# Kernel optimization log

Measured on AMD Instinct MI355X. Metric: run time of the kernel, lower is better.

## Reference

```python
import jax, jax.numpy as jnp
import numpy as np

B, S, D, H = 4, 2048, 1024, 16
HD = D // H  # head_dim = 64


def setup_inputs() -> dict:
    key = jax.random.key(0)
    k_x, k_m, k_wi, k_bi, k_wo, k_bo = jax.random.split(key, 6)
    x = jax.random.normal(k_x, (B, S, D), dtype=jnp.float32)
    mask = jax.random.randint(k_m, (B, S), 0, 2, dtype=jnp.int32)
    # Keras Dense: kernel shape (in, out), glorot-ish scale; bias zeros-ish (random small here)
    w_in = jax.random.normal(k_wi, (D, 3 * D), dtype=jnp.float32) * (1.0 / np.sqrt(D))
    b_in = jax.random.normal(k_bi, (3 * D,), dtype=jnp.float32) * 0.02
    w_out = jax.random.normal(k_wo, (D, D), dtype=jnp.float32) * (1.0 / np.sqrt(D))
    b_out = jax.random.normal(k_bo, (D,), dtype=jnp.float32) * 0.02
    return {"x": x, "w_in": w_in, "b_in": b_in, "w_out": w_out, "b_out": b_out, "mask": mask}


def reference(x, w_in, b_in, w_out, b_out, mask):
    b, s, _ = x.shape
    scale = jnp.asarray(HD ** (-0.5), dtype=x.dtype)
    qkv = x @ w_in + b_in                              # (B, S, 3D)
    qkv = qkv.reshape(b, s, 3, H, HD).transpose(2, 0, 3, 1, 4)  # (3, B, H, S, HD)
    q, k, v = qkv[0], qkv[1], qkv[2]
    q = q * scale
    attn = jnp.einsum("bhqd,bhkd->bhqk", q, k)         # (B, H, S, S)
    neg_inf = jnp.asarray(float("-inf"), dtype=attn.dtype)
    attn_mask = jnp.where(mask[:, None, None, :] > 0, jnp.zeros((), attn.dtype), neg_inf)
    attn = jax.nn.softmax(attn + attn_mask, axis=-1)
    out = jnp.einsum("bhqk,bhkd->bhqd", attn, v)        # (B, H, S, HD)
    out = out.transpose(0, 2, 1, 3).reshape(b, s, D)
    return out @ w_out + b_out
```

## Files before the change

### kernel.cpp

```cpp
#include <hip/hip_runtime.h>

#define B_  4
#define S_  2048
#define D_  1024
#define H_  16
#define HD_ 64
#define BH_ (B_*H_)

typedef _Float16 h16;
typedef _Float16 h4 __attribute__((ext_vector_type(4)));
typedef _Float16 h8 __attribute__((ext_vector_type(8)));
typedef float    f32x4 __attribute__((ext_vector_type(4)));

__device__ __forceinline__ void gload16(const h16* g, h16* l) {
  __builtin_amdgcn_global_load_lds(
      (const __attribute__((address_space(1))) unsigned int*)g,
      (__attribute__((address_space(3))) unsigned int*)l, 16, 0, 0);
}

__global__ void maskscan_k(const int* __restrict__ mask,
                           int* __restrict__ posmap, int* __restrict__ nvalid) {
  __shared__ int partial[256];
  int b = blockIdx.x;
  const int* mb = mask + b * S_;
  int t = threadIdx.x;
  int base = t * 8;
  int loc[8], cnt = 0;
#pragma unroll
  for (int j = 0; j < 8; j++) { loc[j] = cnt; cnt += (mb[base + j] != 0); }
  partial[t] = cnt;
  __syncthreads();
  for (int off = 1; off < 256; off <<= 1) {
    int v = (t >= off) ? partial[t - off] : 0;
    __syncthreads();
    partial[t] += v;
    __syncthreads();
  }
  int excl = (t == 0) ? 0 : partial[t - 1];
#pragma unroll
  for (int j = 0; j < 8; j++)
    posmap[b * S_ + base + j] = (mb[base + j] != 0) ? (excl + loc[j]) : -1;
  if (t == 255) nvalid[b] = partial[255];
}

__global__ void convert_k(const float* __restrict__ in, h16* __restrict__ out,
                          int n) {
  int idx = (blockIdx.x * 256 + threadIdx.x) * 8;
  if (idx + 8 <= n) {
    float4 f0 = *(const float4*)(in + idx);
    float4 f1 = *(const float4*)(in + idx + 4);
    h16 t[8] = {(h16)f0.x, (h16)f0.y, (h16)f0.z, (h16)f0.w,
                (h16)f1.x, (h16)f1.y, (h16)f1.z, (h16)f1.w};
    *(h8*)(out + idx) = *(h8*)t;
  } else {
    for (int j = idx; j < n; j++) out[j] = (h16)in[j];
  }
}

__global__ void transpose_conv_k(const float* __restrict__ in,
                                 h16* __restrict__ out, int R, int C) {
  __shared__ h16 tile[32][33];
  int bx = blockIdx.x * 32;
  int by = blockIdx.y * 32;
  int tx = threadIdx.x, ty = threadIdx.y;
#pragma unroll
  for (int i = 0; i < 32; i += 8)
    tile[ty + i][tx] = (h16)in[(size_t)(by + ty + i) * C + bx + tx];
  __syncthreads();
#pragma unroll
  for (int i = 0; i < 32; i += 8)
    out[(size_t)(bx + ty + i) * R + by + tx] = tile[tx][ty + i];
}

template <int MODE>
__global__ __launch_bounds__(256)
void gemm_bt(const h16* __restrict__ A, const h16* __restrict__ BT,
             const h16* __restrict__ bias, const int* __restrict__ posmap,
             void* __restrict__ out0v, h16* __restrict__ out1,
             h16* __restrict__ out2, int M, int N, int K) {
  const int tid  = threadIdx.x;
  const int lane = tid & 63;
  const int w    = tid >> 6;
  const int quad = lane >> 4;
  const int l16  = lane & 15;
  const int m0   = blockIdx.x * 128;
  const int n0   = blockIdx.y * 128;

  __shared__ alignas(16) h16 As[128 * 32];
  __shared__ alignas(16) h16 Bs[128 * 32];

  const f32x4 zero = {0.f, 0.f, 0.f, 0.f};
  f32x4 acc[4][4];
#pragma unroll
  for (int i = 0; i < 4; i++)
#pragma unroll
    for (int j = 0; j < 4; j++) acc[i][j] = zero;

  const int wm = (w >> 1) * 64;
  const int wn = (w & 1) * 64;
  const int srow = (lane >> 2);
  const int sko  = (lane & 3) * 8;

  for (int kt = 0; kt < K; kt += 32) {
#pragma unroll
    for (int c = 0; c < 2; c++) {
      int chunk = w * 2 + c;
      int row = chunk * 16 + srow;
      gload16(&A[(size_t)(m0 + row) * K + kt + sko], &As[chunk * 512]);
      gload16(&BT[(size_t)(n0 + row) * K + kt + sko], &Bs[chunk * 512]);
    }
    __syncthreads();
    h8 af[4], bfr[4];
#pragma unroll
    for (int i = 0; i < 4; i++)
      af[i] = *(const h8*)(&As[(wm + i * 16 + l16) * 32 + quad * 8]);
#pragma unroll
    for (int j = 0; j < 4; j++)
      bfr[j] = *(const h8*)(&Bs[(wn + j * 16 + l16) * 32 + quad * 8]);
#pragma unroll
    for (int i = 0; i < 4; i++)
#pragma unroll
      for (int j = 0; j < 4; j++)
        acc[i][j] = __builtin_amdgcn_mfma_f32_16x16x32_f16(af[i], bfr[j],
                                                           acc[i][j], 0, 0, 0);
    __syncthreads();
  }

#pragma unroll
  for (int i = 0; i < 4; i++) {
#pragma unroll
    for (int j = 0; j < 4; j++) {
      int n = n0 + wn + j * 16 + l16;
      float bv = (float)bias[n];
#pragma unroll
      for (int r = 0; r < 4; r++) {
        int m = m0 + wm + i * 16 + quad * 4 + r;
        float v = acc[i][j][r] + bv;
        if (MODE == 0) {
          h16* q0 = (h16*)out0v;
          int which = n >> 10;
          int h  = (n >> 6) & 15;
          int hd = n & 63;
          int b  = m >> 11;
          int s  = m & 2047;
          if (which == 0) {
            q0[(((size_t)(b * 16 + h)) * S_ + s) * HD_ + hd] = (h16)(v * 0.125f);
          } else {
            int pos = posmap[b * S_ + s];
            if (pos >= 0) {
              if (which == 1)
                out1[(((size_t)(b * 16 + h)) * S_ + pos) * HD_ + hd] = (h16)v;
              else
                out2[(((size_t)(b * 16 + h)) * HD_ + hd) * S_ + pos] = (h16)v;
            }
          }
        } else {
          ((float*)out0v)[(size_t)m * N + n] = v;
        }
      }
    }
  }
}

__global__ __launch_bounds__(256)
void attn_k(const h16* __restrict__ Q, const h16* __restrict__ Kc,
            const h16* __restrict__ Vtc, const int* __restrict__ nvalid,
            h16* __restrict__ out) {
  const int tid  = threadIdx.x;
  const int lane = tid & 63;
  const int w    = tid >> 6;
  const int quad = lane >> 4;
  const int l16  = lane & 15;
  const int bh   = blockIdx.y;
  const int b    = bh >> 4, h = bh & 15;
  const int q0   = blockIdx.x * 64 + w * 16;
  const int nv   = nvalid[b];

  const h16* Qh = Q   + (size_t)bh * S_ * HD_;
  const h16* Kh = Kc  + (size_t)bh * S_ * HD_;
  const h16* Vh = Vtc + (size_t)bh * HD_ * S_;

  __shared__ alignas(16) h16 Ks[64 * 72];
  __shared__ alignas(16) h16 Vs[64 * 72];
  __shared__ alignas(16) h16 Pb[4][16 * 72];

  h8 bq[2];
#pragma unroll
  for (int ks = 0; ks < 2; ks++)
    bq[ks] = *(const h8*)(&Qh[(size_t)(q0 + l16) * 64 + ks * 32 + quad * 8]);

  const f32x4 zero = {0.f, 0.f, 0.f, 0.f};
  f32x4 oacc[4];
#pragma unroll
  for (int j = 0; j < 4; j++) oacc[j] = zero;
  float mst = -1e30f, lst = 0.f;

  for (int kb = 0; kb < nv; kb += 64) {
    __syncthreads();
#pragma unroll
    for (int pass = 0; pass < 2; pass++) {
      int c = tid + pass * 256;
      int key = c >> 3, ko = (c & 7) * 8;
      *(uint4*)(&Ks[key * 72 + ko]) =
          *(const uint4*)(&Kh[(size_t)(kb + key) * 64 + ko]);
      int hd = c >> 3, vo = (c & 7) * 8;
      *(uint4*)(&Vs[hd * 72 + vo]) =
          *(const uint4*)(&Vh[(size_t)hd * S_ + kb + vo]);
    }
    __syncthreads();

    f32x4 st[4];
#pragma unroll
    for (int kh = 0; kh < 4; kh++) {
      h8 ak0 = *(const h8*)(&Ks[(kh * 16 + l16) * 72 + quad * 8]);
      h8 ak1 = *(const h8*)(&Ks[(kh * 16 + l16) * 72 + 32 + quad * 8]);
      f32x4 s = zero;
      s = __builtin_amdgcn_mfma_f32_16x16x32_f16(ak0, bq[0], s, 0, 0, 0);
      s = __builtin_amdgcn_mfma_f32_16x16x32_f16(ak1, bq[1], s, 0, 0, 0);
      st[kh] = s;
    }
    if (kb + 64 > nv) {
#pragma unroll
      for (int kh = 0; kh < 4; kh++)
#pragma unroll
        for (int r = 0; r < 4; r++)
          if (kb + kh * 16 + quad * 4 + r >= nv) st[kh][r] = -1e30f;
    }

    float mx = -1e30f;
#pragma unroll
    for (int kh = 0; kh < 4; kh++)
#pragma unroll
      for (int r = 0; r < 4; r++) mx = fmaxf(mx, st[kh][r]);
    mx = fmaxf(mx, __shfl_xor(mx, 16, 64));
    mx = fmaxf(mx, __shfl_xor(mx, 32, 64));
    float mnew = fmaxf(mst, mx);
    float alpha = __expf(mst - mnew);
    float p[4][4], rs = 0.f;
#pragma unroll
    for (int kh = 0; kh < 4; kh++)
#pragma unroll
      for (int r = 0; r < 4; r++) {
        p[kh][r] = __expf(st[kh][r] - mnew);
        rs += p[kh][r];
      }
    rs += __shfl_xor(rs, 16, 64);
    rs += __shfl_xor(rs, 32, 64);
    lst = lst * alpha + rs;
    mst = mnew;

    float al[4];
#pragma unroll
    for (int r = 0; r < 4; r++) al[r] = __shfl(alpha, quad * 4 + r, 64);
#pragma unroll
    for (int j = 0; j < 4; j++)
#pragma unroll
      for (int r = 0; r < 4; r++) oacc[j][r] *= al[r];

    h16* pb = Pb[w];
#pragma unroll
    for (int kh = 0; kh < 4; kh++) {
      h4 pk = {(h16)p[kh][0], (h16)p[kh][1], (h16)p[kh][2], (h16)p[kh][3]};
      *(h4*)(&pb[l16 * 72 + kh * 16 + quad * 4]) = pk;
    }
    h8 pa0 = *(const h8*)(&pb[l16 * 72 + quad * 8]);
    h8 pa1 = *(const h8*)(&pb[l16 * 72 + 32 + quad * 8]);

#pragma unroll
    for (int j = 0; j < 4; j++) {
      h8 bv0 = *(const h8*)(&Vs[(j * 16 + l16) * 72 + quad * 8]);
      h8 bv1 = *(const h8*)(&Vs[(j * 16 + l16) * 72 + 32 + quad * 8]);
      oacc[j] = __builtin_amdgcn_mfma_f32_16x16x32_f16(pa0, bv0, oacc[j], 0, 0, 0);
      oacc[j] = __builtin_amdgcn_mfma_f32_16x16x32_f16(pa1, bv1, oacc[j], 0, 0, 0);
    }
  }

  float ls[4];
#pragma unroll
  for (int r = 0; r < 4; r++) ls[r] = __shfl(lst, quad * 4 + r, 64);
#pragma unroll
  for (int j = 0; j < 4; j++)
#pragma unroll
    for (int r = 0; r < 4; r++) {
      int row = q0 + quad * 4 + r;
      float v = oacc[j][r] / ls[r];
      out[((size_t)(b * S_ + row)) * D_ + h * 64 + j * 16 + l16] = (h16)v;
    }
}

extern "C" void kernel_launch(void* const* d_in, const int* in_sizes, int n_in,
                              void* d_out, int out_size, void* d_ws,
                              size_t ws_size, hipStream_t stream) {
  const float* x     = (const float*)d_in[0];
  const float* w_in  = (const float*)d_in[1];
  const float* b_in  = (const float*)d_in[2];
  const float* w_out = (const float*)d_in[3];
  const float* b_out = (const float*)d_in[4];
  const int*   mask  = (const int*)d_in[5];

  const size_t NT = (size_t)BH_ * S_ * HD_;
  h16* ws    = (h16*)d_ws;
  h16* Qb    = ws;
  h16* Kcb   = ws + NT;
  h16* Vtcb  = ws + 2 * NT;
  h16* xc    = ws + 3 * NT;
  h16* AOb   = ws + 3 * NT;
  h16* WouT  = Qb;
  h16* boutc = Vtcb;
  h16* WinT  = (h16*)d_out;
  h16* binc  = (h16*)d_out + 3400704;
  int* posmap = (int*)((char*)d_out + 24u * 1024 * 1024);
  int* nvalid = posmap + B_ * S_;

  maskscan_k<<<B_, 256, 0, stream>>>(mask, posmap, nvalid);
  convert_k<<<2, 256, 0, stream>>>(b_in, binc, 3 * D_);
  transpose_conv_k<<<dim3(3 * D_ / 32, D_ / 32), dim3(32, 8), 0, stream>>>(
      w_in, WinT, D_, 3 * D_);
  convert_k<<<(B_ * S_ * D_) / 2048, 256, 0, stream>>>(x, xc, B_ * S_ * D_);

  gemm_bt<0><<<dim3((B_ * S_) / 128, (3 * D_) / 128), 256, 0, stream>>>(
      xc, WinT, binc, posmap, Qb, Kcb, Vtcb, B_ * S_, 3 * D_, D_);

  attn_k<<<dim3(S_ / 64, BH_), 256, 0, stream>>>(Qb, Kcb, Vtcb, nvalid, AOb);

  transpose_conv_k<<<dim3(D_ / 32, D_ / 32), dim3(32, 8), 0, stream>>>(
      w_out, WouT, D_, D_);
  convert_k<<<1, 256, 0, stream>>>(b_out, boutc, D_);

  gemm_bt<1><<<dim3((B_ * S_) / 128, D_ / 128), 256, 0, stream>>>(
      AOb, WouT, boutc, nullptr, d_out, nullptr, nullptr, B_ * S_, D_, D_);
}
```

Measured before the change: 313.0 us.

## Fuse prep kernels, swizzle LDS with K=64 GEMM tiles, use exp2 softmax

```diff
diff --git a/kernel.cpp b/kernel.cpp
--- a/kernel.cpp
+++ b/kernel.cpp
@@ -6,70 +6,108 @@
 #define H_  16
 #define HD_ 64
 #define BH_ (B_*H_)
+#define QSCALE 0.18033688f
 
 typedef _Float16 h16;
 typedef _Float16 h4 __attribute__((ext_vector_type(4)));
 typedef _Float16 h8 __attribute__((ext_vector_type(8)));
 typedef float    f32x4 __attribute__((ext_vector_type(4)));
 
+#define EXP2(x) __builtin_amdgcn_exp2f(x)
+
 __device__ __forceinline__ void gload16(const h16* g, h16* l) {
   __builtin_amdgcn_global_load_lds(
       (const __attribute__((address_space(1))) unsigned int*)g,
       (__attribute__((address_space(3))) unsigned int*)l, 16, 0, 0);
 }
 
-__global__ void maskscan_k(const int* __restrict__ mask,
-                           int* __restrict__ posmap, int* __restrict__ nvalid) {
-  __shared__ int partial[256];
-  int b = blockIdx.x;
-  const int* mb = mask + b * S_;
+__global__ __launch_bounds__(256)
+void prep_k(const float* __restrict__ x, const float* __restrict__ w_in,
+            const float* __restrict__ b_in, const int* __restrict__ mask,
+            h16* __restrict__ xc, h16* __restrict__ WinT,
+            h16* __restrict__ binc, int* __restrict__ posmap,
+            int* __restrict__ nvalid) {
+  __shared__ __align__(16) char smem[2212];
+  int blk = blockIdx.x;
   int t = threadIdx.x;
-  int base = t * 8;
-  int loc[8], cnt = 0;
-#pragma unroll
-  for (int j = 0; j < 8; j++) { loc[j] = cnt; cnt += (mb[base + j] != 0); }
-  partial[t] = cnt;
-  __syncthreads();
-  for (int off = 1; off < 256; off <<= 1) {
-    int v = (t >= off) ? partial[t - off] : 0;
-    __syncthreads();
-    partial[t] += v;
-    __syncthreads();
-  }
-  int excl = (t == 0) ? 0 : partial[t - 1];
-#pragma unroll
-  for (int j = 0; j < 8; j++)
-    posmap[b * S_ + base + j] = (mb[base + j] != 0) ? (excl + loc[j]) : -1;
-  if (t == 255) nvalid[b] = partial[255];
-}
-
-__global__ void convert_k(const float* __restrict__ in, h16* __restrict__ out,
-                          int n) {
-  int idx = (blockIdx.x * 256 + threadIdx.x) * 8;
-  if (idx + 8 <= n) {
-    float4 f0 = *(const float4*)(in + idx);
-    float4 f1 = *(const float4*)(in + idx + 4);
-    h16 t[8] = {(h16)f0.x, (h16)f0.y, (h16)f0.z, (h16)f0.w,
-                (h16)f1.x, (h16)f1.y, (h16)f1.z, (h16)f1.w};
-    *(h8*)(out + idx) = *(h8*)t;
+  if (blk < 4) {
+    int* partial = (int*)smem;
+    int b = blk;
+    const int* mb = mask + b * S_;
+    int base = t * 8;
+    int loc[8], cnt = 0;
+#pragma unroll
+    for (int j = 0; j < 8; j++) { loc[j] = cnt; cnt += (mb[base + j] != 0); }
+    partial[t] = cnt;
+    __syncthreads();
+    for (int off = 1; off < 256; off <<= 1) {
+      int v = (t >= off) ? partial[t - off] : 0;
+      __syncthreads();
+      partial[t] += v;
+      __syncthreads();
+    }
+    int excl = (t == 0) ? 0 : partial[t - 1];
+#pragma unroll
+    for (int j = 0; j < 8; j++)
+      posmap[b * S_ + base + j] = (mb[base + j] != 0) ? (excl + loc[j]) : -1;
+    if (t == 255) nvalid[b] = partial[255];
+  } else if (blk < 6) {
+    int idx = ((blk - 4) * 256 + t) * 8;
+    if (idx + 8 <= 3 * D_) {
+      float4 f0 = *(const float4*)(b_in + idx);
+      float4 f1 = *(const float4*)(b_in + idx + 4);
+      h16 tmp[8] = {(h16)f0.x, (h16)f0.y, (h16)f0.z, (h16)f0.w,
+                    (h16)f1.x, (h16)f1.y, (h16)f1.z, (h16)f1.w};
+      *(h8*)(binc + idx) = *(h8*)tmp;
+    }
+  } else if (blk < 4102) {
+    int idx = ((blk - 6) * 256 + t) * 8;
+    float4 f0 = *(const float4*)(x + idx);
+    float4 f1 = *(const float4*)(x + idx + 4);
+    h16 tmp[8] = {(h16)f0.x, (h16)f0.y, (h16)f0.z, (h16)f0.w,
+                  (h16)f1.x, (h16)f1.y, (h16)f1.z, (h16)f1.w};
+    *(h8*)(xc + idx) = *(h8*)tmp;
   } else {
-    for (int j = idx; j < n; j++) out[j] = (h16)in[j];
-  }
-}
-
-__global__ void transpose_conv_k(const float* __restrict__ in,
-                                 h16* __restrict__ out, int R, int C) {
+    typedef h16 row33[33];
+    row33* tile = (row33*)smem;
+    int idx = blk - 4102;
+    int bx = (idx % 96) * 32, by = (idx / 96) * 32;
+    int tx = t & 31, ty = t >> 5;
+    const int C = 3 * D_, R = D_;
+#pragma unroll
+    for (int i = 0; i < 32; i += 8)
+      tile[ty + i][tx] = (h16)w_in[(size_t)(by + ty + i) * C + bx + tx];
+    __syncthreads();
+#pragma unroll
+    for (int i = 0; i < 32; i += 8)
+      WinT[(size_t)(bx + ty + i) * R + by + tx] = tile[tx][ty + i];
+  }
+}
+
+__global__ __launch_bounds__(256)
+void post_k(const float* __restrict__ w_out, const float* __restrict__ b_out,
+            h16* __restrict__ WouT, h16* __restrict__ boutc) {
   __shared__ h16 tile[32][33];
-  int bx = blockIdx.x * 32;
-  int by = blockIdx.y * 32;
-  int tx = threadIdx.x, ty = threadIdx.y;
-#pragma unroll
-  for (int i = 0; i < 32; i += 8)
-    tile[ty + i][tx] = (h16)in[(size_t)(by + ty + i) * C + bx + tx];
-  __syncthreads();
-#pragma unroll
-  for (int i = 0; i < 32; i += 8)
-    out[(size_t)(bx + ty + i) * R + by + tx] = tile[tx][ty + i];
+  int blk = blockIdx.x;
+  int t = threadIdx.x;
+  if (blk < 1024) {
+    int bx = (blk % 32) * 32, by = (blk / 32) * 32;
+    int tx = t & 31, ty = t >> 5;
+#pragma unroll
+    for (int i = 0; i < 32; i += 8)
+      tile[ty + i][tx] = (h16)w_out[(size_t)(by + ty + i) * D_ + bx + tx];
+    __syncthreads();
+#pragma unroll
+    for (int i = 0; i < 32; i += 8)
+      WouT[(size_t)(bx + ty + i) * D_ + by + tx] = tile[tx][ty + i];
+  } else {
+    int idx = t * 4;
+    if (idx < D_) {
+      float4 f = *(const float4*)(b_out + idx);
+      h16 tmp[4] = {(h16)f.x, (h16)f.y, (h16)f.z, (h16)f.w};
+      *(h4*)(boutc + idx) = *(h4*)tmp;
+    }
+  }
 }
 
 template <int MODE>
@@ -86,8 +124,8 @@
   const int m0   = blockIdx.x * 128;
   const int n0   = blockIdx.y * 128;
 
-  __shared__ alignas(16) h16 As[128 * 32];
-  __shared__ alignas(16) h16 Bs[128 * 32];
+  __shared__ alignas(16) h16 As[128 * 64];
+  __shared__ alignas(16) h16 Bs[128 * 64];
 
   const f32x4 zero = {0.f, 0.f, 0.f, 0.f};
   f32x4 acc[4][4];
@@ -98,31 +136,38 @@
 
   const int wm = (w >> 1) * 64;
   const int wn = (w & 1) * 64;
-  const int srow = (lane >> 2);
-  const int sko  = (lane & 3) * 8;
-
-  for (int kt = 0; kt < K; kt += 32) {
-#pragma unroll
-    for (int c = 0; c < 2; c++) {
-      int chunk = w * 2 + c;
-      int row = chunk * 16 + srow;
-      gload16(&A[(size_t)(m0 + row) * K + kt + sko], &As[chunk * 512]);
-      gload16(&BT[(size_t)(n0 + row) * K + kt + sko], &Bs[chunk * 512]);
-    }
-    __syncthreads();
-    h8 af[4], bfr[4];
-#pragma unroll
-    for (int i = 0; i < 4; i++)
-      af[i] = *(const h8*)(&As[(wm + i * 16 + l16) * 32 + quad * 8]);
-#pragma unroll
-    for (int j = 0; j < 4; j++)
-      bfr[j] = *(const h8*)(&Bs[(wn + j * 16 + l16) * 32 + quad * 8]);
-#pragma unroll
-    for (int i = 0; i < 4; i++)
+  const int sw = l16 & 7;
+
+  for (int kt = 0; kt < K; kt += 64) {
+#pragma unroll
+    for (int p = 0; p < 4; p++) {
+      int c   = w * 256 + p * 64 + lane;
+      int row = c >> 3;
+      int cc  = (c & 7) ^ (row & 7);
+      gload16(&A[(size_t)(m0 + row) * K + kt + cc * 8],
+              &As[(w * 256 + p * 64) * 8]);
+      gload16(&BT[(size_t)(n0 + row) * K + kt + cc * 8],
+              &Bs[(w * 256 + p * 64) * 8]);
+    }
+    __syncthreads();
+#pragma unroll
+    for (int kk = 0; kk < 2; kk++) {
+      h8 af[4], bfr[4];
+#pragma unroll
+      for (int i = 0; i < 4; i++)
+        af[i] = *(const h8*)(&As[(wm + i * 16 + l16) * 64 +
+                                 ((kk * 4 + quad) ^ sw) * 8]);
 #pragma unroll
       for (int j = 0; j < 4; j++)
-        acc[i][j] = __builtin_amdgcn_mfma_f32_16x16x32_f16(af[i], bfr[j],
-                                                           acc[i][j], 0, 0, 0);
+        bfr[j] = *(const h8*)(&Bs[(wn + j * 16 + l16) * 64 +
+                                  ((kk * 4 + quad) ^ sw) * 8]);
+#pragma unroll
+      for (int i = 0; i < 4; i++)
+#pragma unroll
+        for (int j = 0; j < 4; j++)
+          acc[i][j] = __builtin_amdgcn_mfma_f32_16x16x32_f16(af[i], bfr[j],
+                                                             acc[i][j], 0, 0, 0);
+    }
     __syncthreads();
   }
 
@@ -144,7 +189,7 @@
           int b  = m >> 11;
           int s  = m & 2047;
           if (which == 0) {
-            q0[(((size_t)(b * 16 + h)) * S_ + s) * HD_ + hd] = (h16)(v * 0.125f);
+            q0[(((size_t)(b * 16 + h)) * S_ + s) * HD_ + hd] = (h16)(v * QSCALE);
           } else {
             int pos = posmap[b * S_ + s];
             if (pos >= 0) {
@@ -175,13 +220,14 @@
   const int b    = bh >> 4, h = bh & 15;
   const int q0   = blockIdx.x * 64 + w * 16;
   const int nv   = nvalid[b];
+  const int sw   = l16 & 7;
 
   const h16* Qh = Q   + (size_t)bh * S_ * HD_;
   const h16* Kh = Kc  + (size_t)bh * S_ * HD_;
   const h16* Vh = Vtc + (size_t)bh * HD_ * S_;
 
-  __shared__ alignas(16) h16 Ks[64 * 72];
-  __shared__ alignas(16) h16 Vs[64 * 72];
+  __shared__ alignas(16) h16 Ks[64 * 64];
+  __shared__ alignas(16) h16 Vs[64 * 64];
   __shared__ alignas(16) h16 Pb[4][16 * 72];
 
   h8 bq[2];
@@ -198,22 +244,22 @@
   for (int kb = 0; kb < nv; kb += 64) {
     __syncthreads();
 #pragma unroll
-    for (int pass = 0; pass < 2; pass++) {
-      int c = tid + pass * 256;
-      int key = c >> 3, ko = (c & 7) * 8;
-      *(uint4*)(&Ks[key * 72 + ko]) =
-          *(const uint4*)(&Kh[(size_t)(kb + key) * 64 + ko]);
-      int hd = c >> 3, vo = (c & 7) * 8;
-      *(uint4*)(&Vs[hd * 72 + vo]) =
-          *(const uint4*)(&Vh[(size_t)hd * S_ + kb + vo]);
+    for (int p = 0; p < 2; p++) {
+      int c   = w * 128 + p * 64 + lane;
+      int row = c >> 3;
+      int cc  = (c & 7) ^ (row & 7);
+      gload16(&Kh[(size_t)(kb + row) * 64 + cc * 8],
+              &Ks[(w * 128 + p * 64) * 8]);
+      gload16(&Vh[(size_t)row * S_ + kb + cc * 8],
+              &Vs[(w * 128 + p * 64) * 8]);
     }
     __syncthreads();
 
     f32x4 st[4];
 #pragma unroll
     for (int kh = 0; kh < 4; kh++) {
-      h8 ak0 = *(const h8*)(&Ks[(kh * 16 + l16) * 72 + quad * 8]);
-      h8 ak1 = *(const h8*)(&Ks[(kh * 16 + l16) * 72 + 32 + quad * 8]);
+      h8 ak0 = *(const h8*)(&Ks[(kh * 16 + l16) * 64 + (quad ^ sw) * 8]);
+      h8 ak1 = *(const h8*)(&Ks[(kh * 16 + l16) * 64 + ((quad + 4) ^ sw) * 8]);
       f32x4 s = zero;
       s = __builtin_amdgcn_mfma_f32_16x16x32_f16(ak0, bq[0], s, 0, 0, 0);
       s = __builtin_amdgcn_mfma_f32_16x16x32_f16(ak1, bq[1], s, 0, 0, 0);
@@ -235,13 +281,13 @@
     mx = fmaxf(mx, __shfl_xor(mx, 16, 64));
     mx = fmaxf(mx, __shfl_xor(mx, 32, 64));
     float mnew = fmaxf(mst, mx);
-    float alpha = __expf(mst - mnew);
+    float alpha = EXP2(mst - mnew);
     float p[4][4], rs = 0.f;
 #pragma unroll
     for (int kh = 0; kh < 4; kh++)
 #pragma unroll
       for (int r = 0; r < 4; r++) {
-        p[kh][r] = __expf(st[kh][r] - mnew);
+        p[kh][r] = EXP2(st[kh][r] - mnew);
         rs += p[kh][r];
       }
     rs += __shfl_xor(rs, 16, 64);
@@ -268,8 +314,8 @@
 
 #pragma unroll
     for (int j = 0; j < 4; j++) {
-      h8 bv0 = *(const h8*)(&Vs[(j * 16 + l16) * 72 + quad * 8]);
-      h8 bv1 = *(const h8*)(&Vs[(j * 16 + l16) * 72 + 32 + quad * 8]);
+      h8 bv0 = *(const h8*)(&Vs[(j * 16 + l16) * 64 + (quad ^ sw) * 8]);
+      h8 bv1 = *(const h8*)(&Vs[(j * 16 + l16) * 64 + ((quad + 4) ^ sw) * 8]);
       oacc[j] = __builtin_amdgcn_mfma_f32_16x16x32_f16(pa0, bv0, oacc[j], 0, 0, 0);
       oacc[j] = __builtin_amdgcn_mfma_f32_16x16x32_f16(pa1, bv1, oacc[j], 0, 0, 0);
     }
@@ -312,20 +358,15 @@
   int* posmap = (int*)((char*)d_out + 24u * 1024 * 1024);
   int* nvalid = posmap + B_ * S_;
 
-  maskscan_k<<<B_, 256, 0, stream>>>(mask, posmap, nvalid);
-  convert_k<<<2, 256, 0, stream>>>(b_in, binc, 3 * D_);
-  transpose_conv_k<<<dim3(3 * D_ / 32, D_ / 32), dim3(32, 8), 0, stream>>>(
-      w_in, WinT, D_, 3 * D_);
-  convert_k<<<(B_ * S_ * D_) / 2048, 256, 0, stream>>>(x, xc, B_ * S_ * D_);
+  prep_k<<<7174, 256, 0, stream>>>(x, w_in, b_in, mask, xc, WinT, binc,
+                                   posmap, nvalid);
 
   gemm_bt<0><<<dim3((B_ * S_) / 128, (3 * D_) / 128), 256, 0, stream>>>(
       xc, WinT, binc, posmap, Qb, Kcb, Vtcb, B_ * S_, 3 * D_, D_);
 
   attn_k<<<dim3(S_ / 64, BH_), 256, 0, stream>>>(Qb, Kcb, Vtcb, nvalid, AOb);
 
-  transpose_conv_k<<<dim3(D_ / 32, D_ / 32), dim3(32, 8), 0, stream>>>(
-      w_out, WouT, D_, D_);
-  convert_k<<<1, 256, 0, stream>>>(b_out, boutc, D_);
+  post_k<<<1025, 256, 0, stream>>>(w_out, b_out, WouT, boutc);
 
   gemm_bt<1><<<dim3((B_ * S_) / 128, D_ / 128), 256, 0, stream>>>(
       AOb, WouT, boutc, nullptr, d_out, nullptr, nullptr, B_ * S_, D_, D_);
```

Measured after the change: 298.6 us. 1.05x faster.
